# Optimization experiments

Measured on AMD Instinct MI355X. Metric: run time of the kernel, lower is better.

## Reference

```python
import jax, jax.numpy as jnp
import numpy as np

EMBED_DIM = 512
NUM_HEADS = 8
GAMMA = 0.1


def setup_inputs() -> dict:
    key = jax.random.key(0)
    ks = jax.random.split(key, 16)
    B, T, D, Hp, Wp = 4, 16, EMBED_DIM, 24, 24
    Dq = D // 4
    s = 1.0 / np.sqrt(D)
    inp = {
        "h_opt": jax.random.normal(ks[0], (B, T, D, Hp, Wp), jnp.float32),
        "h_sar": jax.random.normal(ks[1], (B, T, D, Hp, Wp), jnp.float32),
        "Wq": jax.random.normal(ks[2], (D, D), jnp.float32) * s,
        "bq": jnp.zeros((D,), jnp.float32),
        "Wk": jax.random.normal(ks[3], (D, D), jnp.float32) * s,
        "bk": jnp.zeros((D,), jnp.float32),
        "Wv": jax.random.normal(ks[4], (D, D), jnp.float32) * s,
        "bv": jnp.zeros((D,), jnp.float32),
        "Wo": jax.random.normal(ks[5], (D, D), jnp.float32) * s,
        "bo": jnp.zeros((D,), jnp.float32),
        "Wp1": jax.random.normal(ks[6], (D, Dq), jnp.float32) * s,
        "bp1": jnp.zeros((Dq,), jnp.float32),
        "Wp2": jax.random.normal(ks[7], (Dq, 1), jnp.float32) * (1.0 / np.sqrt(Dq)),
        "bp2": jnp.zeros((1,), jnp.float32),
    }
    return inp


def reference(h_opt, h_sar, Wq, bq, Wk, bk, Wv, bv, Wo, bo, Wp1, bp1, Wp2, bp2):
    B, T, D, Hp, Wp_ = h_opt.shape
    S = Hp * Wp_
    H = NUM_HEADS
    hd = D // H

    # (B,T,D,H',W') -> (B*S, T, D): each spatial location is an independent sequence over T
    opt_seq = jnp.transpose(h_opt, (0, 3, 4, 1, 2)).reshape(B * S, T, D)
    sar_seq = jnp.transpose(h_sar, (0, 3, 4, 1, 2)).reshape(B * S, T, D)

    Q = (opt_seq @ Wq + bq).reshape(B * S, T, H, hd)
    K = (sar_seq @ Wk + bk).reshape(B * S, T, H, hd)
    V = (sar_seq @ Wv + bv).reshape(B * S, T, H, hd)

    # scores: (N, H, Tq, Tk)
    scores = jnp.einsum("nthd,nshd->nhts", Q, K) / np.sqrt(hd).astype(np.float32)

    # per-key physical violation penalty: MLP(sar) -> sigmoid in [0,1], shape (N, Tk)
    hdn = jax.nn.gelu(sar_seq @ Wp1 + bp1, approximate=False)
    p_viol = jax.nn.sigmoid((hdn @ Wp2 + bp2).squeeze(-1))  # (N, T)
    scores = scores - GAMMA * p_viol[:, None, None, :]

    attn = jax.nn.softmax(scores, axis=-1)  # dropout is identity in eval mode
    out = jnp.einsum("nhts,nshd->nthd", attn, V).reshape(B * S, T, D)
    out = out @ Wo + bo
    return jnp.transpose(out.reshape(B, Hp, Wp_, T, D), (0, 3, 4, 1, 2))
```

## Files before the change

### kernel.cpp

```cpp
#include <hip/hip_runtime.h>

#define GAMMA 0.1f

typedef unsigned short u16;
typedef u16 u16x8 __attribute__((ext_vector_type(8)));
typedef short s16x8 __attribute__((ext_vector_type(8)));
typedef float f32x4 __attribute__((ext_vector_type(4)));
typedef unsigned int ui32x4 __attribute__((ext_vector_type(4)));

__device__ __forceinline__ float b2f(u16 u) {
  return __uint_as_float(((unsigned)u) << 16);
}
__device__ __forceinline__ u16 f2bf(float f) {
  unsigned u = __float_as_uint(f);
  unsigned r = (u + 0x7FFFu + ((u >> 16) & 1u)) >> 16;
  return (u16)r;
}
__device__ __forceinline__ unsigned pk_bf16(float lo, float hi) {
  return (unsigned)f2bf(lo) | ((unsigned)f2bf(hi) << 16);
}

__device__ __forceinline__ void gl2lds16(const u16* g, u16* l) {
  __builtin_amdgcn_global_load_lds(
      (const __attribute__((address_space(1))) unsigned int*)g,
      (__attribute__((address_space(3))) unsigned int*)l, 16, 0, 0);
}

__device__ __forceinline__ int xcd_swz(int phys, int nwg) {
  return (phys & 7) * (nwg >> 3) + (phys >> 3);
}

__global__ __launch_bounds__(256) void transpose_k(
    const float* __restrict__ src, u16* __restrict__ dst, int K, int N)
{
  int idx = blockIdx.x * 256 + threadIdx.x;
  if (idx >= K * N) return;
  int nn = idx / K, kk = idx - nn * K;
  dst[idx] = f2bf(src[kk * N + nn]);
}

__global__ __launch_bounds__(256) void bias_kernel(
    const float* __restrict__ bq, const float* __restrict__ bk,
    const float* __restrict__ bv, const float* __restrict__ bp1,
    const float* __restrict__ bo,
    float* __restrict__ biasQ, float* __restrict__ biasKVP,
    float* __restrict__ biasO)
{
  int i = blockIdx.x * 256 + threadIdx.x;
  if (i < 512) {
    biasQ[i] = bq[i];
  } else if (i < 1664) {
    int j = i - 512;
    float v;
    if (j < 512) v = bk[j];
    else if (j < 1024) v = bv[j - 512];
    else v = bp1[j - 1024];
    biasKVP[j] = v;
  } else if (i < 2176) {
    biasO[i - 1664] = bo[i - 1664];
  }
}

__global__ __launch_bounds__(256) void gemm_gather(
    const float* __restrict__ h, const u16* __restrict__ WT,
    const float* __restrict__ bias, u16* __restrict__ C, int NC)
{
  __shared__ __align__(16) u16 Al[64 * 64];
  __shared__ __align__(16) u16 Bl[2][128 * 64];
  const int tid = threadIdx.x;
  const int w = tid >> 6, lane = tid & 63;
  const int lhi = lane >> 4, llo = lane & 15;

  const int nwg = gridDim.x * gridDim.y;
  const int phys = blockIdx.y * gridDim.x + blockIdx.x;
  const int logical = xcd_swz(phys, nwg);
  const int bx = logical % gridDim.x;
  const int y = logical / gridDim.x;

  const int bt = y / 9, stile = y - bt * 9;
  const int s0 = stile * 64;
  const int col0 = bx * 128;

  const float* Ab = h + (size_t)bt * (512 * 576) + s0;
  const u16* Bb = WT + (size_t)col0 * 512;

  const int s_a = tid & 63;
  const int c_a = tid >> 6;
  const int sw_a = s_a & 7;
  const float* apb = Ab + s_a;

  const int brow = lane >> 3;
  const int bko = ((lane & 7) ^ brow) * 8;

  f32x4 acc[4][2];
#pragma unroll
  for (int mi = 0; mi < 4; ++mi)
#pragma unroll
    for (int ni = 0; ni < 2; ++ni)
#pragma unroll
      for (int e = 0; e < 4; ++e) acc[mi][ni][e] = 0.f;

  float pre[16];
#pragma unroll
  for (int i = 0; i < 4; ++i) {
    int q = w * 4 + i;
    gl2lds16(Bb + (size_t)(q * 8 + brow) * 512 + bko, &Bl[0][q * 512]);
  }
#pragma unroll
  for (int j = 0; j < 8; ++j) pre[j] = apb[(size_t)(c_a * 8 + j) * 576];
#pragma unroll
  for (int j = 0; j < 8; ++j) pre[8 + j] = apb[(size_t)(c_a * 8 + 32 + j) * 576];

  for (int kt = 0; kt < 8; ++kt) {
    unsigned cw[8];
#pragma unroll
    for (int i = 0; i < 4; ++i) {
      cw[i]     = pk_bf16(pre[2 * i],     pre[2 * i + 1]);
      cw[4 + i] = pk_bf16(pre[8 + 2 * i], pre[9 + 2 * i]);
    }
    __syncthreads();
    {
      ui32x4 v0 = {cw[0], cw[1], cw[2], cw[3]};
      ui32x4 v1 = {cw[4], cw[5], cw[6], cw[7]};
      *(ui32x4*)&Al[s_a * 64 + ((c_a ^ sw_a) * 8)] = v0;
      *(ui32x4*)&Al[s_a * 64 + (((c_a + 4) ^ sw_a) * 8)] = v1;
    }
    __syncthreads();

    if (kt < 7) {
      const int ktn = kt + 1;
#pragma unroll
      for (int i = 0; i < 4; ++i) {
        int q = w * 4 + i;
        gl2lds16(Bb + (size_t)(q * 8 + brow) * 512 + ktn * 64 + bko,
                 &Bl[ktn & 1][q * 512]);
      }
#pragma unroll
      for (int j = 0; j < 8; ++j)
        pre[j] = apb[(size_t)(ktn * 64 + c_a * 8 + j) * 576];
#pragma unroll
      for (int j = 0; j < 8; ++j)
        pre[8 + j] = apb[(size_t)(ktn * 64 + c_a * 8 + 32 + j) * 576];
    }

    const u16* Blc = Bl[kt & 1];
#pragma unroll
    for (int hh = 0; hh < 2; ++hh) {
      s16x8 af[4], bfr[2];
#pragma unroll
      for (int mi = 0; mi < 4; ++mi) {
        int row = mi * 16 + llo;
        af[mi] = *(const s16x8*)&Al[row * 64 + ((((hh << 2) | lhi) ^ (row & 7)) * 8)];
      }
#pragma unroll
      for (int ni = 0; ni < 2; ++ni) {
        int n = w * 32 + ni * 16 + llo;
        bfr[ni] = *(const s16x8*)&Blc[n * 64 + ((((hh << 2) | lhi) ^ (n & 7)) * 8)];
      }
#pragma unroll
      for (int mi = 0; mi < 4; ++mi)
#pragma unroll
        for (int ni = 0; ni < 2; ++ni)
          acc[mi][ni] = __builtin_amdgcn_mfma_f32_16x16x32_bf16(
              af[mi], bfr[ni], acc[mi][ni], 0, 0, 0);
    }
  }

  const int b_ = bt >> 4, t_ = bt & 15;
  const size_t rowbase = (size_t)(b_ * 576 + s0) * 16 + t_;
  float bia0 = bias[col0 + w * 32 + llo];
  float bia1 = bias[col0 + w * 32 + 16 + llo];
#pragma unroll
  for (int mi = 0; mi < 4; ++mi) {
#pragma unroll
    for (int i = 0; i < 4; ++i) {
      const int m = mi * 16 + lhi * 4 + i;
      u16* cp = C + (rowbase + (size_t)m * 16) * NC + col0 + w * 32 + llo;
      cp[0]  = f2bf(acc[mi][0][i] + bia0);
      cp[16] = f2bf(acc[mi][1][i] + bia1);
    }
  }
}

__global__ __launch_bounds__(256) void pviol_kernel(
    const u16* __restrict__ KVP, const float* __restrict__ Wp2,
    const float* __restrict__ bp2, float* __restrict__ pv)
{
  const int tid = threadIdx.x;
  const int w = tid >> 6, lane = tid & 63;
  const int row = blockIdx.x * 4 + w;
  const int c = lane * 2;
  const u16* hp = KVP + (size_t)row * 1152 + 1024 + c;
  float x0 = b2f(hp[0]), x1 = b2f(hp[1]);
  float g0 = 0.5f * x0 * (1.f + erff(x0 * 0.70710678f));
  float g1 = 0.5f * x1 * (1.f + erff(x1 * 0.70710678f));
  float sum = g0 * Wp2[c] + g1 * Wp2[c + 1];
#pragma unroll
  for (int d = 1; d < 64; d <<= 1) sum += __shfl_xor(sum, d, 64);
  if (lane == 0) {
    float z = sum + bp2[0];
    pv[row] = 1.f / (1.f + expf(-z));
  }
}

__global__ __launch_bounds__(256) void attn_kernel(
    const u16* Q, const u16* __restrict__ KVP,
    const float* __restrict__ pviol, u16* att)
{
  __shared__ __align__(16) u16 Kl[4][16 * 72];
  __shared__ __align__(16) u16 Vl[4][16 * 72];
  __shared__ float Pl[4][16 * 17];
  const int tid = threadIdx.x;
  const int w = tid >> 6, lane = tid & 63;
  const int logical = xcd_swz(blockIdx.x, gridDim.x);
  const int wid = logical * 4 + w;
  const int n = wid >> 3, hh = wid & 7;
  const int g = lane >> 4, tq = lane & 15;

  const int r = lane >> 3, co = (lane & 7) * 8;
  const u16* Kb = KVP + (size_t)n * (16 * 1152) + hh * 64;
#pragma unroll
  for (int rr = 0; rr < 2; ++rr) {
    int row = r + rr * 8;
    *(u16x8*)&Kl[w][row * 72 + co] = *(const u16x8*)(Kb + row * 1152 + co);
    *(u16x8*)&Vl[w][row * 72 + co] = *(const u16x8*)(Kb + 512 + row * 1152 + co);
  }
  __syncthreads();

  float s[4] = {0.f, 0.f, 0.f, 0.f};
  const u16* Qr = Q + ((size_t)n * 16 + tq) * 512 + hh * 64;
  for (int kc = 0; kc < 8; ++kc) {
    u16x8 q8 = *(const u16x8*)(Qr + kc * 8);
    float qf[8];
#pragma unroll
    for (int j = 0; j < 8; ++j) qf[j] = b2f(q8[j]);
#pragma unroll
    for (int i = 0; i < 4; ++i) {
      u16x8 k8 = *(const u16x8*)&Kl[w][(g * 4 + i) * 72 + kc * 8];
#pragma unroll
      for (int j = 0; j < 8; ++j) s[i] += qf[j] * b2f(k8[j]);
    }
  }

  const float* pv = pviol + n * 16;
#pragma unroll
  for (int i = 0; i < 4; ++i) s[i] = s[i] * 0.125f - GAMMA * pv[g * 4 + i];

  float mx = fmaxf(fmaxf(s[0], s[1]), fmaxf(s[2], s[3]));
  mx = fmaxf(mx, __shfl_xor(mx, 16, 64));
  mx = fmaxf(mx, __shfl_xor(mx, 32, 64));
  float e[4], sum = 0.f;
#pragma unroll
  for (int i = 0; i < 4; ++i) { e[i] = expf(s[i] - mx); sum += e[i]; }
  sum += __shfl_xor(sum, 16, 64);
  sum += __shfl_xor(sum, 32, 64);
  float inv = 1.f / sum;
#pragma unroll
  for (int i = 0; i < 4; ++i) Pl[w][tq * 17 + g * 4 + i] = e[i] * inv;
  __syncthreads();

  float o[16];
#pragma unroll
  for (int j = 0; j < 16; ++j) o[j] = 0.f;
  for (int tk = 0; tk < 16; ++tk) {
    float p = Pl[w][tq * 17 + tk];
    u16x8 v0 = *(const u16x8*)&Vl[w][tk * 72 + g * 16];
    u16x8 v1 = *(const u16x8*)&Vl[w][tk * 72 + g * 16 + 8];
#pragma unroll
    for (int j = 0; j < 8; ++j) {
      o[j]     += p * b2f(v0[j]);
      o[8 + j] += p * b2f(v1[j]);
    }
  }
  u16* op = att + ((size_t)n * 16 + tq) * 512 + hh * 64 + g * 16;
  u16x8 r0, r1;
#pragma unroll
  for (int j = 0; j < 8; ++j) { r0[j] = f2bf(o[j]); r1[j] = f2bf(o[8 + j]); }
  *(u16x8*)op = r0;
  *(u16x8*)(op + 8) = r1;
}

__global__ __launch_bounds__(256) void gemm_out(
    const u16* __restrict__ A, const u16* __restrict__ WT,
    const float* __restrict__ bias, float* __restrict__ out)
{
  __shared__ __align__(16) char smem[49152];
  u16* Al0 = (u16*)smem;
  u16* Bl0 = (u16*)(smem + 16384);
  const int tid = threadIdx.x;
  const int w = tid >> 6, lane = tid & 63;
  const int lhi = lane >> 4, llo = lane & 15;

  const int nwg = gridDim.x * gridDim.y;
  const int phys = blockIdx.y * gridDim.x + blockIdx.x;
  const int logical = xcd_swz(phys, nwg);
  const int bx = logical % gridDim.x;
  const int y = logical / gridDim.x;

  const int bt = y / 9, stile = y - bt * 9;
  const int s0 = stile * 64;
  const int col0 = bx * 128;
  const int b_ = bt >> 4, t_ = bt & 15;

  const u16* Ab = A + ((size_t)(b_ * 576 + s0) * 16 + t_) * 512;
  const u16* Bb = WT + (size_t)col0 * 512;

  const int brow = lane >> 3;
  const int bko = ((lane & 7) ^ brow) * 8;

  f32x4 acc[4][2];
#pragma unroll
  for (int mi = 0; mi < 4; ++mi)
#pragma unroll
    for (int ni = 0; ni < 2; ++ni)
#pragma unroll
      for (int e = 0; e < 4; ++e) acc[mi][ni][e] = 0.f;

#pragma unroll
  for (int i = 0; i < 2; ++i) {
    int q = w * 2 + i;
    gl2lds16(Ab + (size_t)(q * 8 + brow) * (16 * 512) + bko, &Al0[q * 512]);
  }
#pragma unroll
  for (int i = 0; i < 4; ++i) {
    int q = w * 4 + i;
    gl2lds16(Bb + (size_t)(q * 8 + brow) * 512 + bko, &Bl0[q * 512]);
  }

  for (int kt = 0; kt < 8; ++kt) {
    __syncthreads();
    if (kt < 7) {
      const int ktn = kt + 1;
      u16* Ala = Al0 + (ktn & 1) * (64 * 64);
      u16* Bla = Bl0 + (ktn & 1) * (128 * 64);
#pragma unroll
      for (int i = 0; i < 2; ++i) {
        int q = w * 2 + i;
        gl2lds16(Ab + (size_t)(q * 8 + brow) * (16 * 512) + ktn * 64 + bko,
                 &Ala[q * 512]);
      }
#pragma unroll
      for (int i = 0; i < 4; ++i) {
        int q = w * 4 + i;
        gl2lds16(Bb + (size_t)(q * 8 + brow) * 512 + ktn * 64 + bko,
                 &Bla[q * 512]);
      }
    }
    const u16* Alc = Al0 + (kt & 1) * (64 * 64);
    const u16* Blc = Bl0 + (kt & 1) * (128 * 64);
#pragma unroll
    for (int hh = 0; hh < 2; ++hh) {
      s16x8 af[4], bfr[2];
#pragma unroll
      for (int mi = 0; mi < 4; ++mi) {
        int row = mi * 16 + llo;
        af[mi] = *(const s16x8*)&Alc[row * 64 + ((((hh << 2) | lhi) ^ (row & 7)) * 8)];
      }
#pragma unroll
      for (int ni = 0; ni < 2; ++ni) {
        int n = w * 32 + ni * 16 + llo;
        bfr[ni] = *(const s16x8*)&Blc[n * 64 + ((((hh << 2) | lhi) ^ (n & 7)) * 8)];
      }
#pragma unroll
      for (int mi = 0; mi < 4; ++mi)
#pragma unroll
        for (int ni = 0; ni < 2; ++ni)
          acc[mi][ni] = __builtin_amdgcn_mfma_f32_16x16x32_bf16(
              af[mi], bfr[ni], acc[mi][ni], 0, 0, 0);
    }
  }

  __syncthreads();
  float* Cl = (float*)smem;
  float bia0 = bias[col0 + w * 32 + llo];
  float bia1 = bias[col0 + w * 32 + 16 + llo];
#pragma unroll
  for (int mi = 0; mi < 4; ++mi)
#pragma unroll
    for (int i = 0; i < 4; ++i) {
      int m = mi * 16 + lhi * 4 + i;
      Cl[(w * 32 + llo) * 72 + m]      = acc[mi][0][i] + bia0;
      Cl[(w * 32 + 16 + llo) * 72 + m] = acc[mi][1][i] + bia1;
    }
  __syncthreads();
  const int nn = tid >> 1;
  const int mh = (tid & 1) * 32;
  const float* sp = Cl + nn * 72 + mh;
  float* dp = out + ((size_t)bt * 512 + col0 + nn) * 576 + s0 + mh;
#pragma unroll
  for (int j = 0; j < 8; ++j)
    *(float4*)(dp + j * 4) = *(const float4*)(sp + j * 4);
}

extern "C" void kernel_launch(void* const* d_in, const int* in_sizes, int n_in,
                              void* d_out, int out_size, void* d_ws, size_t ws_size,
                              hipStream_t stream)
{
  const float* h_opt = (const float*)d_in[0];
  const float* h_sar = (const float*)d_in[1];
  const float* Wq  = (const float*)d_in[2];
  const float* bq  = (const float*)d_in[3];
  const float* Wk  = (const float*)d_in[4];
  const float* bk  = (const float*)d_in[5];
  const float* Wv  = (const float*)d_in[6];
  const float* bv  = (const float*)d_in[7];
  const float* Wo  = (const float*)d_in[8];
  const float* bo  = (const float*)d_in[9];
  const float* Wp1 = (const float*)d_in[10];
  const float* bp1 = (const float*)d_in[11];
  const float* Wp2 = (const float*)d_in[12];
  const float* bp2 = (const float*)d_in[13];
  float* out = (float*)d_out;

  char* ws = (char*)d_ws;
  u16*   WqT     = (u16*)(ws + 0);
  u16*   KVPW    = (u16*)(ws + 524288);
  u16*   WoT     = (u16*)(ws + 1703936);
  float* biasQ   = (float*)(ws + 2228224);
  float* biasKVP = (float*)(ws + 2230272);
  float* biasO   = (float*)(ws + 2234880);
  float* pviol   = (float*)(ws + 2236928);
  u16*   Qbuf    = (u16*)(ws + 2384384);
  u16*   KVPbuf  = (u16*)(ws + 40133120);

  transpose_k<<<1024, 256, 0, stream>>>(Wq, WqT, 512, 512);
  transpose_k<<<1024, 256, 0, stream>>>(Wk, KVPW, 512, 512);
  transpose_k<<<1024, 256, 0, stream>>>(Wv, KVPW + 512 * 512, 512, 512);
  transpose_k<<<256, 256, 0, stream>>>(Wp1, KVPW + 1024 * 512, 512, 128);
  transpose_k<<<1024, 256, 0, stream>>>(Wo, WoT, 512, 512);
  bias_kernel<<<9, 256, 0, stream>>>(bq, bk, bv, bp1, bo, biasQ, biasKVP, biasO);

  gemm_gather<<<dim3(4, 576), 256, 0, stream>>>(h_opt, WqT, biasQ, Qbuf, 512);
  gemm_gather<<<dim3(9, 576), 256, 0, stream>>>(h_sar, KVPW, biasKVP, KVPbuf, 1152);
  pviol_kernel<<<9216, 256, 0, stream>>>(KVPbuf, Wp2, bp2, pviol);
  attn_kernel<<<4608, 256, 0, stream>>>(Qbuf, KVPbuf, pviol, Qbuf);
  gemm_out<<<dim3(4, 576), 256, 0, stream>>>(Qbuf, WoT, biasO, out);
}
```

Measured before the change: 421.4 us.

## Pre-convert inputs to transposed bf16 and async-load A tiles in projection GEMM

Adds a convert_h kernel that turns h_opt and h_sar from fp32 into bf16 and transposes them into an S-major layout in workspace. The projection GEMM then streams its A tiles through double-buffered global_load_lds, the same way it loads the weights, instead of doing strided fp32 loads, packing in registers and storing to LDS. This removes per-tile conversion work and a barrier from the GEMM loop and stops the K/V/P GEMM from re-reading the fp32 h_sar once per column block. The cost is an extra full pass over both inputs (an fp32 read plus a bf16 write) and more workspace.

```diff
diff --git a/kernel.cpp b/kernel.cpp
--- a/kernel.cpp
+++ b/kernel.cpp
@@ -61,11 +61,44 @@
   }
 }
 
-__global__ __launch_bounds__(256) void gemm_gather(
-    const float* __restrict__ h, const u16* __restrict__ WT,
+__global__ __launch_bounds__(256) void convert_h(
+    const float* __restrict__ h0, const float* __restrict__ h1,
+    u16* __restrict__ d0, u16* __restrict__ d1)
+{
+  __shared__ __align__(16) u16 T[64 * 64];
+  const int tid = threadIdx.x;
+  const int kt = blockIdx.x & 7, st = blockIdx.x >> 3;
+  const int bt = blockIdx.y;
+  const float* src = (blockIdx.z ? h1 : h0) + (size_t)bt * (512 * 576);
+  u16* dst = (blockIdx.z ? d1 : d0) + (size_t)bt * (576 * 512);
+
+  const int s = tid & 63, kc = tid >> 6;
+  const float* sp = src + (size_t)(kt * 64 + kc * 16) * 576 + st * 64 + s;
+  unsigned pk[8];
+#pragma unroll
+  for (int i = 0; i < 8; ++i) {
+    float lo = sp[(2 * i) * 576];
+    float hi = sp[(2 * i + 1) * 576];
+    pk[i] = pk_bf16(lo, hi);
+  }
+  ui32x4 v0 = {pk[0], pk[1], pk[2], pk[3]};
+  ui32x4 v1 = {pk[4], pk[5], pk[6], pk[7]};
+  *(ui32x4*)&T[s * 64 + (((kc * 2)     ^ (s & 7)) * 8)] = v0;
+  *(ui32x4*)&T[s * 64 + (((kc * 2 + 1) ^ (s & 7)) * 8)] = v1;
+  __syncthreads();
+  const int r = tid >> 2, oc = (tid & 3) * 2;
+  ui32x4 w0 = *(const ui32x4*)&T[r * 64 + ((oc       ^ (r & 7)) * 8)];
+  ui32x4 w1 = *(const ui32x4*)&T[r * 64 + (((oc + 1) ^ (r & 7)) * 8)];
+  u16* dp = dst + (size_t)(st * 64 + r) * 512 + kt * 64 + oc * 8;
+  *(ui32x4*)dp = w0;
+  *(ui32x4*)(dp + 8) = w1;
+}
+
+__global__ __launch_bounds__(256) void gemm_proj(
+    const u16* __restrict__ hT, const u16* __restrict__ WT,
     const float* __restrict__ bias, u16* __restrict__ C, int NC)
 {
-  __shared__ __align__(16) u16 Al[64 * 64];
+  __shared__ __align__(16) u16 Al[2][64 * 64];
   __shared__ __align__(16) u16 Bl[2][128 * 64];
   const int tid = threadIdx.x;
   const int w = tid >> 6, lane = tid & 63;
@@ -81,13 +114,8 @@
   const int s0 = stile * 64;
   const int col0 = bx * 128;
 
-  const float* Ab = h + (size_t)bt * (512 * 576) + s0;
+  const u16* Ab = hT + (size_t)bt * (576 * 512) + (size_t)s0 * 512;
   const u16* Bb = WT + (size_t)col0 * 512;
-
-  const int s_a = tid & 63;
-  const int c_a = tid >> 6;
-  const int sw_a = s_a & 7;
-  const float* apb = Ab + s_a;
 
   const int brow = lane >> 3;
   const int bko = ((lane & 7) ^ brow) * 8;
@@ -100,49 +128,35 @@
 #pragma unroll
       for (int e = 0; e < 4; ++e) acc[mi][ni][e] = 0.f;
 
-  float pre[16];
+#pragma unroll
+  for (int i = 0; i < 2; ++i) {
+    int q = w * 2 + i;
+    gl2lds16(Ab + (size_t)(q * 8 + brow) * 512 + bko, &Al[0][q * 512]);
+  }
 #pragma unroll
   for (int i = 0; i < 4; ++i) {
     int q = w * 4 + i;
     gl2lds16(Bb + (size_t)(q * 8 + brow) * 512 + bko, &Bl[0][q * 512]);
   }
-#pragma unroll
-  for (int j = 0; j < 8; ++j) pre[j] = apb[(size_t)(c_a * 8 + j) * 576];
-#pragma unroll
-  for (int j = 0; j < 8; ++j) pre[8 + j] = apb[(size_t)(c_a * 8 + 32 + j) * 576];
 
   for (int kt = 0; kt < 8; ++kt) {
-    unsigned cw[8];
-#pragma unroll
-    for (int i = 0; i < 4; ++i) {
-      cw[i]     = pk_bf16(pre[2 * i],     pre[2 * i + 1]);
-      cw[4 + i] = pk_bf16(pre[8 + 2 * i], pre[9 + 2 * i]);
-    }
     __syncthreads();
-    {
-      ui32x4 v0 = {cw[0], cw[1], cw[2], cw[3]};
-      ui32x4 v1 = {cw[4], cw[5], cw[6], cw[7]};
-      *(ui32x4*)&Al[s_a * 64 + ((c_a ^ sw_a) * 8)] = v0;
-      *(ui32x4*)&Al[s_a * 64 + (((c_a + 4) ^ sw_a) * 8)] = v1;
-    }
-    __syncthreads();
-
     if (kt < 7) {
       const int ktn = kt + 1;
+#pragma unroll
+      for (int i = 0; i < 2; ++i) {
+        int q = w * 2 + i;
+        gl2lds16(Ab + (size_t)(q * 8 + brow) * 512 + ktn * 64 + bko,
+                 &Al[ktn & 1][q * 512]);
+      }
 #pragma unroll
       for (int i = 0; i < 4; ++i) {
         int q = w * 4 + i;
         gl2lds16(Bb + (size_t)(q * 8 + brow) * 512 + ktn * 64 + bko,
                  &Bl[ktn & 1][q * 512]);
       }
-#pragma unroll
-      for (int j = 0; j < 8; ++j)
-        pre[j] = apb[(size_t)(ktn * 64 + c_a * 8 + j) * 576];
-#pragma unroll
-      for (int j = 0; j < 8; ++j)
-        pre[8 + j] = apb[(size_t)(ktn * 64 + c_a * 8 + 32 + j) * 576];
-    }
-
+    }
+    const u16* Alc = Al[kt & 1];
     const u16* Blc = Bl[kt & 1];
 #pragma unroll
     for (int hh = 0; hh < 2; ++hh) {
@@ -150,7 +164,7 @@
 #pragma unroll
       for (int mi = 0; mi < 4; ++mi) {
         int row = mi * 16 + llo;
-        af[mi] = *(const s16x8*)&Al[row * 64 + ((((hh << 2) | lhi) ^ (row & 7)) * 8)];
+        af[mi] = *(const s16x8*)&Alc[row * 64 + ((((hh << 2) | lhi) ^ (row & 7)) * 8)];
       }
 #pragma unroll
       for (int ni = 0; ni < 2; ++ni) {
@@ -422,6 +436,8 @@
   float* pviol   = (float*)(ws + 2236928);
   u16*   Qbuf    = (u16*)(ws + 2384384);
   u16*   KVPbuf  = (u16*)(ws + 40133120);
+  u16*   hTopt   = (u16*)(ws + 125067776);
+  u16*   hTsar   = (u16*)(ws + 162816512);
 
   transpose_k<<<1024, 256, 0, stream>>>(Wq, WqT, 512, 512);
   transpose_k<<<1024, 256, 0, stream>>>(Wk, KVPW, 512, 512);
@@ -429,9 +445,10 @@
   transpose_k<<<256, 256, 0, stream>>>(Wp1, KVPW + 1024 * 512, 512, 128);
   transpose_k<<<1024, 256, 0, stream>>>(Wo, WoT, 512, 512);
   bias_kernel<<<9, 256, 0, stream>>>(bq, bk, bv, bp1, bo, biasQ, biasKVP, biasO);
-
-  gemm_gather<<<dim3(4, 576), 256, 0, stream>>>(h_opt, WqT, biasQ, Qbuf, 512);
-  gemm_gather<<<dim3(9, 576), 256, 0, stream>>>(h_sar, KVPW, biasKVP, KVPbuf, 1152);
+  convert_h<<<dim3(72, 64, 2), 256, 0, stream>>>(h_opt, h_sar, hTopt, hTsar);
+
+  gemm_proj<<<dim3(4, 576), 256, 0, stream>>>(hTopt, WqT, biasQ, Qbuf, 512);
+  gemm_proj<<<dim3(9, 576), 256, 0, stream>>>(hTsar, KVPW, biasKVP, KVPbuf, 1152);
   pviol_kernel<<<9216, 256, 0, stream>>>(KVPbuf, Wp2, bp2, pviol);
   attn_kernel<<<4608, 256, 0, stream>>>(Qbuf, KVPbuf, pviol, Qbuf);
   gemm_out<<<dim3(4, 576), 256, 0, stream>>>(Qbuf, WoT, biasO, out);
```

Result: no change. 427.3 us (+1.4%).
